# Optimization experiments

Hardware: AMD Instinct MI355X
Metric: run time of the kernel (lower is better)

Reference implementation:

```python
import jax, jax.numpy as jnp
import numpy as np

B, S, D = 2, 2048, 2048
H, KVH = 32, 8
HD = D // H          # 64
N_REP = H // KVH     # 4
NEG = -1e9


def setup_inputs() -> dict:
    key = jax.random.key(0)
    ks = jax.random.split(key, 5)
    x = jax.random.normal(ks[0], (B, S, D), dtype=jnp.float32)
    std = 0.02
    wq = jax.random.normal(ks[1], (H * HD, D), dtype=jnp.float32) * std
    wk = jax.random.normal(ks[2], (KVH * HD, D), dtype=jnp.float32) * std
    wv = jax.random.normal(ks[3], (KVH * HD, D), dtype=jnp.float32) * std
    wo = jax.random.normal(ks[4], (D, H * HD), dtype=jnp.float32) * std
    # RoPE tables: (S, HD//2)
    inv_freq = 1.0 / (10000.0 ** (np.arange(0, HD, 2, dtype=np.float32) / HD))
    t = np.arange(S, dtype=np.float32)
    freqs = np.outer(t, inv_freq)
    freqs_cos = jnp.asarray(np.cos(freqs))
    freqs_sin = jnp.asarray(np.sin(freqs))
    # additive causal mask [1,1,S,S]
    causal = np.tril(np.ones((S, S), dtype=bool))
    mask = jnp.asarray(np.where(causal, 0.0, NEG).astype(np.float32))[None, None]
    return {"x": x, "wq": wq, "wk": wk, "wv": wv, "wo": wo,
            "freqs_cos": freqs_cos, "freqs_sin": freqs_sin, "mask": mask}


def _apply_rope(t, cos, sin):
    # t: [B,S,nh,HD]; cos/sin: [S, HD//2]
    tr = t.reshape(t.shape[:-1] + (HD // 2, 2))
    r, i = tr[..., 0], tr[..., 1]
    c = cos[None, :, None, :]
    s = sin[None, :, None, :]
    out_r = r * c - i * s
    out_i = r * s + i * c
    return jnp.stack([out_r, out_i], axis=-1).reshape(t.shape)


def reference(x, wq, wk, wv, wo, freqs_cos, freqs_sin, mask):
    b, s, _ = x.shape
    q = (x @ wq.T).reshape(b, s, H, HD)
    k = (x @ wk.T).reshape(b, s, KVH, HD)
    v = (x @ wv.T).reshape(b, s, KVH, HD)
    q = _apply_rope(q, freqs_cos, freqs_sin)
    k = _apply_rope(k, freqs_cos, freqs_sin)
    # repeat_kv (GQA expansion) then move heads forward: [B,H,S,HD]
    k = jnp.repeat(k, N_REP, axis=2)
    v = jnp.repeat(v, N_REP, axis=2)
    q = q.transpose(0, 2, 1, 3)
    k = k.transpose(0, 2, 1, 3)
    v = v.transpose(0, 2, 1, 3)
    scale = 1.0 / jnp.sqrt(jnp.float32(HD))
    scores = jnp.einsum("bhqd,bhkd->bhqk", q, k) * scale + mask[:, :, :s, :s]
    attn = jax.nn.softmax(scores, axis=-1)
    out = jnp.einsum("bhqk,bhkd->bhqd", attn, v)
    out = out.transpose(0, 2, 1, 3).reshape(b, s, H * HD)
    return out @ wo.T
```

## Files before the change

### kernel.cpp

```cpp
#include <hip/hip_runtime.h>
#include <hip/hip_bf16.h>
#include <stdint.h>


#define NEG_BIG (-1e9f)
#define SCALE_LOG2 0.18033688011112042f

typedef __bf16 bf16x8 __attribute__((ext_vector_type(8)));
typedef float f32x4 __attribute__((ext_vector_type(4)));
typedef float f32x16 __attribute__((ext_vector_type(16)));
typedef uint16_t u16x8 __attribute__((ext_vector_type(8)));
typedef uint32_t u32x4 __attribute__((ext_vector_type(4)));

__device__ inline uint16_t f2bf(float x) {
    __hip_bfloat16 h = __float2bfloat16(x);
    return __builtin_bit_cast(uint16_t, h);
}
__device__ inline float bf2f(uint16_t u) {
    uint32_t t = (uint32_t)u << 16;
    return __builtin_bit_cast(float, t);
}

__device__ inline void async_cp16(const void* g, void* l) {
    __builtin_amdgcn_global_load_lds(
        (const __attribute__((address_space(1))) uint32_t*)g,
        (__attribute__((address_space(3))) uint32_t*)l,
        16 , 0 , 0 );
}

__global__ void cvt4(const float* __restrict__ in, uint16_t* __restrict__ out, int n4) {
    int i = blockIdx.x * blockDim.x + threadIdx.x;
    if (i >= n4) return;
    const float4 v = ((const float4*)in)[i];
    ushort4 o;
    o.x = f2bf(v.x); o.y = f2bf(v.y); o.z = f2bf(v.z); o.w = f2bf(v.w);
    ((ushort4*)out)[i] = o;
}

__global__ void build_wqkv(const float* __restrict__ wq, const float* __restrict__ wk,
                           const float* __restrict__ wv, uint16_t* __restrict__ out) {
    int i = blockIdx.x * blockDim.x + threadIdx.x;
    if (i >= (3072 * 2048) / 4) return;
    int e = i * 4;
    int row = e >> 11;
    int col = e & 2047;
    const float* src = (row < 2048) ? (wq + (long)row * 2048 + col)
                     : (row < 2560) ? (wk + (long)(row - 2048) * 2048 + col)
                                    : (wv + (long)(row - 2560) * 2048 + col);
    const float4 v = *(const float4*)src;
    ushort4 o;
    o.x = f2bf(v.x); o.y = f2bf(v.y); o.z = f2bf(v.z); o.w = f2bf(v.w);
    ((ushort4*)(out + e))[0] = o;
}

template <int OUT_BF16>
__global__ __launch_bounds__(256) void gemm_bt(const uint16_t* __restrict__ A,
                                               const uint16_t* __restrict__ Bw,
                                               void* __restrict__ Cout,
                                               int M, int N, int K) {
    __shared__ __align__(16) uint16_t Asm[128 * 32];
    __shared__ __align__(16) uint16_t Bsm[128 * 32];
    const int t = threadIdx.x;
    const int l = t & 63;
    const int w = t >> 6;
    const int wr = w >> 1, wc = w & 1;
    const int c = l & 15, g = l >> 4;
    const long row0 = (long)blockIdx.x * 128;
    const long col0 = (long)blockIdx.y * 128;

    f32x4 acc[4][4] = {};

    const uint16_t* aSrc = A + (row0 + (t >> 2)) * (long)K + (t & 3) * 8;
    const uint16_t* bSrc = Bw + (col0 + (t >> 2)) * (long)K + (t & 3) * 8;
    const long half = 64L * K;

    for (int k0 = 0; k0 < K; k0 += 32) {
        __syncthreads();
        async_cp16(aSrc + k0, &Asm[t * 8]);
        async_cp16(aSrc + half + k0, &Asm[2048 + t * 8]);
        async_cp16(bSrc + k0, &Bsm[t * 8]);
        async_cp16(bSrc + half + k0, &Bsm[2048 + t * 8]);
        __syncthreads();

        bf16x8 aF[4], bF[4];
        const int ko = g * 8;
#pragma unroll
        for (int m = 0; m < 4; ++m)
            aF[m] = *(const bf16x8*)&Asm[(wr * 64 + m * 16 + c) * 32 + ko];
#pragma unroll
        for (int n = 0; n < 4; ++n)
            bF[n] = *(const bf16x8*)&Bsm[(wc * 64 + n * 16 + c) * 32 + ko];
#pragma unroll
        for (int m = 0; m < 4; ++m)
#pragma unroll
            for (int n = 0; n < 4; ++n)
                acc[m][n] = __builtin_amdgcn_mfma_f32_16x16x32_bf16(aF[m], bF[n], acc[m][n], 0, 0, 0);
    }

#pragma unroll
    for (int m = 0; m < 4; ++m) {
        const long rg = row0 + wr * 64 + m * 16 + g * 4;
#pragma unroll
        for (int n = 0; n < 4; ++n) {
            const long cg = col0 + wc * 64 + n * 16 + c;
#pragma unroll
            for (int r = 0; r < 4; ++r) {
                float v = acc[m][n][r];
                if (OUT_BF16)
                    ((uint16_t*)Cout)[(rg + r) * (long)N + cg] = f2bf(v);
                else
                    ((float*)Cout)[(rg + r) * (long)N + cg] = v;
            }
        }
    }
}

__global__ void rope_inplace(uint16_t* __restrict__ qkv,
                             const float* __restrict__ cosT,
                             const float* __restrict__ sinT) {
    const int PPR = 1280;
    int idx = blockIdx.x * blockDim.x + threadIdx.x;
    if (idx >= 4096 * PPR) return;
    int m = idx / PPR;
    int j = idx - m * PPR;
    int col = (j < 1024) ? (2 * j) : (2048 + 2 * (j - 1024));
    int s = m & 2047;
    int d2 = j & 31;
    float cc = cosT[s * 32 + d2];
    float ss = sinT[s * 32 + d2];
    uint32_t* p = (uint32_t*)(qkv + (long)m * 3072 + col);
    uint32_t v = *p;
    float re = bf2f((uint16_t)(v & 0xffffu));
    float im = bf2f((uint16_t)(v >> 16));
    float orr = re * cc - im * ss;
    float oi = re * ss + im * cc;
    *p = (uint32_t)f2bf(orr) | ((uint32_t)f2bf(oi) << 16);
}

__global__ void pack_vt(const uint16_t* __restrict__ qkv, uint16_t* __restrict__ Vt) {
    const int wid = (blockIdx.x * blockDim.x + threadIdx.x) >> 6;
    const int lane = threadIdx.x & 63;
    const int head = wid >> 8;
    const int sblk = wid & 255;
    const int b = head >> 3, kvh = head & 7;
    const uint16_t* src = qkv + ((long)(b * 2048 + sblk * 8)) * 3072 + 2560 + kvh * 64 + lane;
    u16x8 v;
#pragma unroll
    for (int j = 0; j < 8; ++j) v[j] = src[(long)j * 3072];
    uint16_t* dst = Vt + ((long)head * 64 + lane) * 2048 + sblk * 8;
    *(u16x8*)dst = v;
}

__global__ void kpack(const uint16_t* __restrict__ qkv, uint16_t* __restrict__ Kpk) {
    const int wid = (blockIdx.x * blockDim.x + threadIdx.x) >> 6;
    const int l = threadIdx.x & 63;
    const int lq = l & 31, hi = l >> 5;
    const int s = wid & 3;
    const int tile = (wid >> 2) & 63;
    const int bk = wid >> 8;
    const int b = bk >> 3, kvh = bk & 7;
    const uint16_t* src = qkv + (long)(b * 2048 + 32 * tile + lq) * 3072
                        + 2048 + kvh * 64 + 16 * s + 8 * hi;
    u16x8 v = *(const u16x8*)src;
    *(u16x8*)(Kpk + (((long)(bk * 64 + tile) * 4 + s) * 64 + l) * 8) = v;
}

__global__ void vpack2(const uint16_t* __restrict__ Vt, uint16_t* __restrict__ Vpk) {
    const int wid = (blockIdx.x * blockDim.x + threadIdx.x) >> 6;
    const int l = threadIdx.x & 63;
    const int lq = l & 31, hi = l >> 5;
    const int s2 = wid & 1;
    const int nd = (wid >> 1) & 1;
    const int tile = (wid >> 2) & 63;
    const int bk = wid >> 8;
    const uint16_t* src = Vt + ((long)(bk * 64 + nd * 32 + lq)) * 2048
                        + 32 * tile + 16 * s2 + 8 * hi;
    u16x8 v = *(const u16x8*)src;
    *(u16x8*)(Vpk + ((((long)(bk * 64 + tile) * 2 + nd) * 2 + s2) * 64 + l) * 8) = v;
}

__global__ __launch_bounds__(128, 4) void attn_fwd(const uint16_t* __restrict__ qkv,
                                                   const uint16_t* __restrict__ Kpk,
                                                   const uint16_t* __restrict__ Vpk,
                                                   uint16_t* __restrict__ outb) {
    const int bid = blockIdx.x;
    const int bhp = bid & 31;
    const int j = 63 - (bid >> 5);
    const int t = threadIdx.x;
    const int l = t & 63, ww = t >> 6;
    const int gh = 2 * bhp + ww;
    const int b = gh >> 5, h = gh & 31;
    const int kvh = h >> 2;
    const int bk = b * 8 + kvh;
    const int lq = l & 31, hi = l >> 5;
    const int q = 32 * j + lq;

    const uint16_t* qrow = qkv + (long)(b * 2048 + q) * 3072 + h * 64 + 8 * hi;
    bf16x8 qf[4];
#pragma unroll
    for (int s = 0; s < 4; ++s) qf[s] = *(const bf16x8*)(qrow + 16 * s);

    float m_run = -1e30f, l_run = 0.f;
    f32x16 accO[2] = {};

    const uint16_t* kbase = Kpk + (long)bk * 64 * 2048 + (long)l * 8;
    const uint16_t* vbase = Vpk + (long)bk * 64 * 2048 + (long)l * 8;
    const int ntiles = j + 1;

    for (int tile = 0; tile < ntiles; ++tile) {
        const uint16_t* kp = kbase + (long)tile * 2048;
        bf16x8 kf[4];
#pragma unroll
        for (int s = 0; s < 4; ++s) kf[s] = *(const bf16x8*)(kp + s * 512);

        f32x16 st = {};
#pragma unroll
        for (int s = 0; s < 4; ++s)
            st = __builtin_amdgcn_mfma_f32_32x32x16_bf16(kf[s], qf[s], st, 0, 0, 0);

        const uint16_t* vp = vbase + (long)tile * 2048;
        bf16x8 vf[2][2];
#pragma unroll
        for (int nd = 0; nd < 2; ++nd)
#pragma unroll
            for (int s2 = 0; s2 < 2; ++s2)
                vf[nd][s2] = *(const bf16x8*)(vp + nd * 1024 + s2 * 512);

        float sc[16];
        if (tile == j) {
            const int tq = lq - 4 * hi;
#pragma unroll
            for (int r = 0; r < 16; ++r) {
                const int kc = (r & 3) + 8 * (r >> 2);
                sc[r] = st[r] * SCALE_LOG2 + (kc > tq ? NEG_BIG : 0.f);
            }
        } else {
#pragma unroll
            for (int r = 0; r < 16; ++r) sc[r] = st[r] * SCALE_LOG2;
        }

        float vm = sc[0];
#pragma unroll
        for (int r = 1; r < 16; ++r) vm = fmaxf(vm, sc[r]);
        vm = fmaxf(vm, __shfl_xor(vm, 32));
        const float mnew = fmaxf(m_run, vm);
        const float alpha = __builtin_amdgcn_exp2f(m_run - mnew);
        m_run = mnew;

        float pr[16];
        float sum = 0.f;
#pragma unroll
        for (int r = 0; r < 16; ++r) {
            pr[r] = __builtin_amdgcn_exp2f(sc[r] - mnew);
            sum += pr[r];
        }
        sum += __shfl_xor(sum, 32);
        l_run = l_run * alpha + sum;

        uint32_t wds[8], xw[8];
#pragma unroll
        for (int m = 0; m < 8; ++m)
            wds[m] = (uint32_t)f2bf(pr[2 * m]) | ((uint32_t)f2bf(pr[2 * m + 1]) << 16);
#pragma unroll
        for (int m = 0; m < 8; ++m)
            xw[m] = (uint32_t)__shfl_xor((int)wds[m], 32);

        bf16x8 pf[2];
#pragma unroll
        for (int s = 0; s < 2; ++s) {
            u32x4 pk;
            pk[0] = hi ? xw[4 * s + 2] : wds[4 * s + 0];
            pk[1] = hi ? xw[4 * s + 3] : wds[4 * s + 1];
            pk[2] = hi ? wds[4 * s + 2] : xw[4 * s + 0];
            pk[3] = hi ? wds[4 * s + 3] : xw[4 * s + 1];
            pf[s] = __builtin_bit_cast(bf16x8, pk);
        }

#pragma unroll
        for (int nd = 0; nd < 2; ++nd)
#pragma unroll
            for (int r = 0; r < 16; ++r) accO[nd][r] *= alpha;
#pragma unroll
        for (int nd = 0; nd < 2; ++nd)
#pragma unroll
            for (int s = 0; s < 2; ++s)
                accO[nd] = __builtin_amdgcn_mfma_f32_32x32x16_bf16(vf[nd][s], pf[s], accO[nd], 0, 0, 0);
    }

    const float invl = 1.0f / l_run;
    uint16_t* orow = outb + (long)(b * 2048 + q) * 2048 + h * 64 + 4 * hi;
#pragma unroll
    for (int nd = 0; nd < 2; ++nd)
#pragma unroll
        for (int m = 0; m < 4; ++m) {
            ushort4 o;
            o.x = f2bf(accO[nd][4 * m + 0] * invl);
            o.y = f2bf(accO[nd][4 * m + 1] * invl);
            o.z = f2bf(accO[nd][4 * m + 2] * invl);
            o.w = f2bf(accO[nd][4 * m + 3] * invl);
            *(ushort4*)(orow + nd * 32 + 8 * m) = o;
        }
}

extern "C" void kernel_launch(void* const* d_in, const int* in_sizes, int n_in,
                              void* d_out, int out_size, void* d_ws, size_t ws_size,
                              hipStream_t stream) {
    const float* x    = (const float*)d_in[0];
    const float* wq   = (const float*)d_in[1];
    const float* wk   = (const float*)d_in[2];
    const float* wv   = (const float*)d_in[3];
    const float* wo   = (const float*)d_in[4];
    const float* fcos = (const float*)d_in[5];
    const float* fsin = (const float*)d_in[6];
    float* out = (float*)d_out;

    uint8_t* ws = (uint8_t*)d_ws;
    const size_t MiB = 1048576;
    uint16_t* x_bf   = (uint16_t*)(ws);
    uint16_t* w_bf   = (uint16_t*)(ws + 16 * MiB);
    uint16_t* qkv_bf = (uint16_t*)(ws + 28 * MiB);
    uint16_t* att_bf = x_bf;
    uint16_t* Kpk    = (uint16_t*)(ws + 16 * MiB);
    uint16_t* Vpk    = (uint16_t*)(ws + 20 * MiB);
    uint16_t* Vt     = (uint16_t*)(ws + 24 * MiB);
    uint16_t* wo_bf  = (uint16_t*)(ws + 16 * MiB);

    cvt4<<<(2097152 + 255) / 256, 256, 0, stream>>>(x, x_bf, 2097152);
    build_wqkv<<<(1572864 + 255) / 256, 256, 0, stream>>>(wq, wk, wv, w_bf);

    gemm_bt<1><<<dim3(32, 24), 256, 0, stream>>>(x_bf, w_bf, qkv_bf, 4096, 3072, 2048);

    rope_inplace<<<(4096 * 1280 + 255) / 256, 256, 0, stream>>>(qkv_bf, fcos, fsin);

    pack_vt<<<1024, 256, 0, stream>>>(qkv_bf, Vt);
    kpack<<<1024, 256, 0, stream>>>(qkv_bf, Kpk);
    vpack2<<<1024, 256, 0, stream>>>(Vt, Vpk);

    attn_fwd<<<2048, 128, 0, stream>>>(qkv_bf, Kpk, Vpk, att_bf);

    cvt4<<<(1048576 + 255) / 256, 256, 0, stream>>>(wo, wo_bf, 1048576);
    gemm_bt<0><<<dim3(32, 16), 256, 0, stream>>>(att_bf, wo_bf, out, 4096, 2048, 2048);
}
```

Baseline: 236.7 us.

## Fuse K RoPE into packing, pack V directly, unroll attention two tiles with deferred rescale

K RoPE now runs inside the K packing kernel and V is packed straight from the qkv buffer, which drops the Vt intermediate and one launch. The attention loop handles two 32-key tiles per iteration and raises MFMA wave priority with s_setprio. It skips the online-softmax rescale unless the new max exceeds the running max by a threshold. The unroll raises register pressure, and the launch_bounds occupancy hint is removed. The deferred rescale lets exponentials reach up to 2^10 before the bf16 cast, which may shift precision.

```diff
diff --git a/kernel.cpp b/kernel.cpp
--- a/kernel.cpp
+++ b/kernel.cpp
@@ -5,6 +5,7 @@
 
 #define NEG_BIG (-1e9f)
 #define SCALE_LOG2 0.18033688011112042f
+#define DEFER_THR 10.0f
 
 typedef __bf16 bf16x8 __attribute__((ext_vector_type(8)));
 typedef float f32x4 __attribute__((ext_vector_type(4)));
@@ -115,20 +116,18 @@
     }
 }
 
-__global__ void rope_inplace(uint16_t* __restrict__ qkv,
-                             const float* __restrict__ cosT,
-                             const float* __restrict__ sinT) {
-    const int PPR = 1280;
+__global__ void rope_q(uint16_t* __restrict__ qkv,
+                       const float* __restrict__ cosT,
+                       const float* __restrict__ sinT) {
     int idx = blockIdx.x * blockDim.x + threadIdx.x;
-    if (idx >= 4096 * PPR) return;
-    int m = idx / PPR;
-    int j = idx - m * PPR;
-    int col = (j < 1024) ? (2 * j) : (2048 + 2 * (j - 1024));
+    if (idx >= 4096 * 1024) return;
+    int m = idx >> 10;
+    int j = idx & 1023;
     int s = m & 2047;
     int d2 = j & 31;
     float cc = cosT[s * 32 + d2];
     float ss = sinT[s * 32 + d2];
-    uint32_t* p = (uint32_t*)(qkv + (long)m * 3072 + col);
+    uint32_t* p = (uint32_t*)(qkv + (long)m * 3072 + 2 * j);
     uint32_t v = *p;
     float re = bf2f((uint16_t)(v & 0xffffu));
     float im = bf2f((uint16_t)(v >> 16));
@@ -137,21 +136,10 @@
     *p = (uint32_t)f2bf(orr) | ((uint32_t)f2bf(oi) << 16);
 }
 
-__global__ void pack_vt(const uint16_t* __restrict__ qkv, uint16_t* __restrict__ Vt) {
-    const int wid = (blockIdx.x * blockDim.x + threadIdx.x) >> 6;
-    const int lane = threadIdx.x & 63;
-    const int head = wid >> 8;
-    const int sblk = wid & 255;
-    const int b = head >> 3, kvh = head & 7;
-    const uint16_t* src = qkv + ((long)(b * 2048 + sblk * 8)) * 3072 + 2560 + kvh * 64 + lane;
-    u16x8 v;
-#pragma unroll
-    for (int j = 0; j < 8; ++j) v[j] = src[(long)j * 3072];
-    uint16_t* dst = Vt + ((long)head * 64 + lane) * 2048 + sblk * 8;
-    *(u16x8*)dst = v;
-}
-
-__global__ void kpack(const uint16_t* __restrict__ qkv, uint16_t* __restrict__ Kpk) {
+__global__ void kpack_rope(const uint16_t* __restrict__ qkv,
+                           const float* __restrict__ cosT,
+                           const float* __restrict__ sinT,
+                           uint16_t* __restrict__ Kpk) {
     const int wid = (blockIdx.x * blockDim.x + threadIdx.x) >> 6;
     const int l = threadIdx.x & 63;
     const int lq = l & 31, hi = l >> 5;
@@ -159,13 +147,25 @@
     const int tile = (wid >> 2) & 63;
     const int bk = wid >> 8;
     const int b = bk >> 3, kvh = bk & 7;
-    const uint16_t* src = qkv + (long)(b * 2048 + 32 * tile + lq) * 3072
+    const int key = 32 * tile + lq;
+    const uint16_t* src = qkv + (long)(b * 2048 + key) * 3072
                         + 2048 + kvh * 64 + 16 * s + 8 * hi;
     u16x8 v = *(const u16x8*)src;
-    *(u16x8*)(Kpk + (((long)(bk * 64 + tile) * 4 + s) * 64 + l) * 8) = v;
-}
-
-__global__ void vpack2(const uint16_t* __restrict__ Vt, uint16_t* __restrict__ Vpk) {
+    const int d2b = 8 * s + 4 * hi;
+    u16x8 o;
+#pragma unroll
+    for (int p = 0; p < 4; ++p) {
+        const float cc = cosT[key * 32 + d2b + p];
+        const float ss = sinT[key * 32 + d2b + p];
+        const float re = bf2f(v[2 * p]);
+        const float im = bf2f(v[2 * p + 1]);
+        o[2 * p]     = f2bf(re * cc - im * ss);
+        o[2 * p + 1] = f2bf(re * ss + im * cc);
+    }
+    *(u16x8*)(Kpk + (((long)(bk * 64 + tile) * 4 + s) * 64 + l) * 8) = o;
+}
+
+__global__ void vpack_direct(const uint16_t* __restrict__ qkv, uint16_t* __restrict__ Vpk) {
     const int wid = (blockIdx.x * blockDim.x + threadIdx.x) >> 6;
     const int l = threadIdx.x & 63;
     const int lq = l & 31, hi = l >> 5;
@@ -173,21 +173,44 @@
     const int nd = (wid >> 1) & 1;
     const int tile = (wid >> 2) & 63;
     const int bk = wid >> 8;
-    const uint16_t* src = Vt + ((long)(bk * 64 + nd * 32 + lq)) * 2048
-                        + 32 * tile + 16 * s2 + 8 * hi;
-    u16x8 v = *(const u16x8*)src;
+    const int b = bk >> 3, kvh = bk & 7;
+    const int key0 = 32 * tile + 16 * s2 + 8 * hi;
+    const uint16_t* src = qkv + (long)(b * 2048 + key0) * 3072
+                        + 2560 + kvh * 64 + nd * 32 + lq;
+    u16x8 v;
+#pragma unroll
+    for (int jj = 0; jj < 8; ++jj) v[jj] = src[(long)jj * 3072];
     *(u16x8*)(Vpk + ((((long)(bk * 64 + tile) * 2 + nd) * 2 + s2) * 64 + l) * 8) = v;
 }
 
-__global__ __launch_bounds__(128, 4) void attn_fwd(const uint16_t* __restrict__ qkv,
-                                                   const uint16_t* __restrict__ Kpk,
-                                                   const uint16_t* __restrict__ Vpk,
-                                                   uint16_t* __restrict__ outb) {
+__device__ inline void pack_pf(const float pr[16], int hi, bf16x8 pf[2]) {
+    uint32_t wds[8], xw[8];
+#pragma unroll
+    for (int m = 0; m < 8; ++m)
+        wds[m] = (uint32_t)f2bf(pr[2 * m]) | ((uint32_t)f2bf(pr[2 * m + 1]) << 16);
+#pragma unroll
+    for (int m = 0; m < 8; ++m)
+        xw[m] = (uint32_t)__shfl_xor((int)wds[m], 32);
+#pragma unroll
+    for (int s = 0; s < 2; ++s) {
+        u32x4 pk;
+        pk[0] = hi ? xw[4 * s + 2] : wds[4 * s + 0];
+        pk[1] = hi ? xw[4 * s + 3] : wds[4 * s + 1];
+        pk[2] = hi ? wds[4 * s + 2] : xw[4 * s + 0];
+        pk[3] = hi ? wds[4 * s + 3] : xw[4 * s + 1];
+        pf[s] = __builtin_bit_cast(bf16x8, pk);
+    }
+}
+
+__global__ __launch_bounds__(128) void attn_fwd(const uint16_t* __restrict__ qkv,
+                                                const uint16_t* __restrict__ Kpk,
+                                                const uint16_t* __restrict__ Vpk,
+                                                uint16_t* __restrict__ outb) {
     const int bid = blockIdx.x;
     const int bhp = bid & 31;
     const int j = 63 - (bid >> 5);
-    const int t = threadIdx.x;
-    const int l = t & 63, ww = t >> 6;
+    const int t0 = threadIdx.x;
+    const int l = t0 & 63, ww = t0 >> 6;
     const int gh = 2 * bhp + ww;
     const int b = gh >> 5, h = gh & 31;
     const int kvh = h >> 2;
@@ -205,86 +228,98 @@
 
     const uint16_t* kbase = Kpk + (long)bk * 64 * 2048 + (long)l * 8;
     const uint16_t* vbase = Vpk + (long)bk * 64 * 2048 + (long)l * 8;
-    const int ntiles = j + 1;
-
-    for (int tile = 0; tile < ntiles; ++tile) {
-        const uint16_t* kp = kbase + (long)tile * 2048;
-        bf16x8 kf[4];
-#pragma unroll
-        for (int s = 0; s < 4; ++s) kf[s] = *(const bf16x8*)(kp + s * 512);
-
-        f32x16 st = {};
+    const int nT = (j + 2) >> 1;
+
+    for (int t = 0; t < nT; ++t) {
+        bf16x8 kf[2][4];
+#pragma unroll
+        for (int u = 0; u < 2; ++u)
+#pragma unroll
+            for (int s = 0; s < 4; ++s)
+                kf[u][s] = *(const bf16x8*)(kbase + (long)(2 * t + u) * 2048 + s * 512);
+
+        f32x16 st0 = {}, st1 = {};
+        __builtin_amdgcn_s_setprio(1);
 #pragma unroll
         for (int s = 0; s < 4; ++s)
-            st = __builtin_amdgcn_mfma_f32_32x32x16_bf16(kf[s], qf[s], st, 0, 0, 0);
-
-        const uint16_t* vp = vbase + (long)tile * 2048;
-        bf16x8 vf[2][2];
-#pragma unroll
-        for (int nd = 0; nd < 2; ++nd)
-#pragma unroll
-            for (int s2 = 0; s2 < 2; ++s2)
-                vf[nd][s2] = *(const bf16x8*)(vp + nd * 1024 + s2 * 512);
-
-        float sc[16];
-        if (tile == j) {
-            const int tq = lq - 4 * hi;
+            st0 = __builtin_amdgcn_mfma_f32_32x32x16_bf16(kf[0][s], qf[s], st0, 0, 0, 0);
+#pragma unroll
+        for (int s = 0; s < 4; ++s)
+            st1 = __builtin_amdgcn_mfma_f32_32x32x16_bf16(kf[1][s], qf[s], st1, 0, 0, 0);
+        __builtin_amdgcn_s_setprio(0);
+
+        bf16x8 vf[2][2][2];
+#pragma unroll
+        for (int u = 0; u < 2; ++u)
+#pragma unroll
+            for (int nd = 0; nd < 2; ++nd)
+#pragma unroll
+                for (int s2 = 0; s2 < 2; ++s2)
+                    vf[u][nd][s2] = *(const bf16x8*)(vbase + (long)(2 * t + u) * 2048 + nd * 1024 + s2 * 512);
+
+        float sc0[16], sc1[16];
+        if (t == nT - 1) {
+            const int tq0 = lq + ((j - 2 * t) << 5) - 4 * hi;
+            const int tq1 = tq0 - 32;
 #pragma unroll
             for (int r = 0; r < 16; ++r) {
                 const int kc = (r & 3) + 8 * (r >> 2);
-                sc[r] = st[r] * SCALE_LOG2 + (kc > tq ? NEG_BIG : 0.f);
+                sc0[r] = st0[r] * SCALE_LOG2 + (kc > tq0 ? NEG_BIG : 0.f);
+                sc1[r] = st1[r] * SCALE_LOG2 + (kc > tq1 ? NEG_BIG : 0.f);
             }
         } else {
 #pragma unroll
-            for (int r = 0; r < 16; ++r) sc[r] = st[r] * SCALE_LOG2;
-        }
-
-        float vm = sc[0];
-#pragma unroll
-        for (int r = 1; r < 16; ++r) vm = fmaxf(vm, sc[r]);
+            for (int r = 0; r < 16; ++r) {
+                sc0[r] = st0[r] * SCALE_LOG2;
+                sc1[r] = st1[r] * SCALE_LOG2;
+            }
+        }
+
+        float vm = sc0[0];
+#pragma unroll
+        for (int r = 1; r < 16; ++r) vm = fmaxf(vm, sc0[r]);
+#pragma unroll
+        for (int r = 0; r < 16; ++r) vm = fmaxf(vm, sc1[r]);
         vm = fmaxf(vm, __shfl_xor(vm, 32));
-        const float mnew = fmaxf(m_run, vm);
-        const float alpha = __builtin_amdgcn_exp2f(m_run - mnew);
-        m_run = mnew;
-
-        float pr[16];
+        if (!__all(vm - m_run <= DEFER_THR)) {
+            const float mnew = fmaxf(m_run, vm);
+            const float alpha = __builtin_amdgcn_exp2f(m_run - mnew);
+            m_run = mnew;
+            l_run *= alpha;
+#pragma unroll
+            for (int nd = 0; nd < 2; ++nd)
+#pragma unroll
+                for (int r = 0; r < 16; ++r) accO[nd][r] *= alpha;
+        }
+
+        float pr0[16], pr1[16];
         float sum = 0.f;
 #pragma unroll
         for (int r = 0; r < 16; ++r) {
-            pr[r] = __builtin_amdgcn_exp2f(sc[r] - mnew);
-            sum += pr[r];
+            pr0[r] = __builtin_amdgcn_exp2f(sc0[r] - m_run);
+            sum += pr0[r];
+        }
+#pragma unroll
+        for (int r = 0; r < 16; ++r) {
+            pr1[r] = __builtin_amdgcn_exp2f(sc1[r] - m_run);
+            sum += pr1[r];
         }
         sum += __shfl_xor(sum, 32);
-        l_run = l_run * alpha + sum;
-
-        uint32_t wds[8], xw[8];
-#pragma unroll
-        for (int m = 0; m < 8; ++m)
-            wds[m] = (uint32_t)f2bf(pr[2 * m]) | ((uint32_t)f2bf(pr[2 * m + 1]) << 16);
-#pragma unroll
-        for (int m = 0; m < 8; ++m)
-            xw[m] = (uint32_t)__shfl_xor((int)wds[m], 32);
-
-        bf16x8 pf[2];
-#pragma unroll
-        for (int s = 0; s < 2; ++s) {
-            u32x4 pk;
-            pk[0] = hi ? xw[4 * s + 2] : wds[4 * s + 0];
-            pk[1] = hi ? xw[4 * s + 3] : wds[4 * s + 1];
-            pk[2] = hi ? wds[4 * s + 2] : xw[4 * s + 0];
-            pk[3] = hi ? wds[4 * s + 3] : xw[4 * s + 1];
-            pf[s] = __builtin_bit_cast(bf16x8, pk);
-        }
-
-#pragma unroll
-        for (int nd = 0; nd < 2; ++nd)
-#pragma unroll
-            for (int r = 0; r < 16; ++r) accO[nd][r] *= alpha;
-#pragma unroll
-        for (int nd = 0; nd < 2; ++nd)
-#pragma unroll
-            for (int s = 0; s < 2; ++s)
-                accO[nd] = __builtin_amdgcn_mfma_f32_32x32x16_bf16(vf[nd][s], pf[s], accO[nd], 0, 0, 0);
+        l_run += sum;
+
+        bf16x8 pf0[2], pf1[2];
+        pack_pf(pr0, hi, pf0);
+        pack_pf(pr1, hi, pf1);
+
+        __builtin_amdgcn_s_setprio(1);
+#pragma unroll
+        for (int nd = 0; nd < 2; ++nd) {
+            accO[nd] = __builtin_amdgcn_mfma_f32_32x32x16_bf16(vf[0][nd][0], pf0[0], accO[nd], 0, 0, 0);
+            accO[nd] = __builtin_amdgcn_mfma_f32_32x32x16_bf16(vf[0][nd][1], pf0[1], accO[nd], 0, 0, 0);
+            accO[nd] = __builtin_amdgcn_mfma_f32_32x32x16_bf16(vf[1][nd][0], pf1[0], accO[nd], 0, 0, 0);
+            accO[nd] = __builtin_amdgcn_mfma_f32_32x32x16_bf16(vf[1][nd][1], pf1[1], accO[nd], 0, 0, 0);
+        }
+        __builtin_amdgcn_s_setprio(0);
     }
 
     const float invl = 1.0f / l_run;
@@ -322,7 +357,6 @@
     uint16_t* att_bf = x_bf;
     uint16_t* Kpk    = (uint16_t*)(ws + 16 * MiB);
     uint16_t* Vpk    = (uint16_t*)(ws + 20 * MiB);
-    uint16_t* Vt     = (uint16_t*)(ws + 24 * MiB);
     uint16_t* wo_bf  = (uint16_t*)(ws + 16 * MiB);
 
     cvt4<<<(2097152 + 255) / 256, 256, 0, stream>>>(x, x_bf, 2097152);
@@ -330,11 +364,9 @@
 
     gemm_bt<1><<<dim3(32, 24), 256, 0, stream>>>(x_bf, w_bf, qkv_bf, 4096, 3072, 2048);
 
-    rope_inplace<<<(4096 * 1280 + 255) / 256, 256, 0, stream>>>(qkv_bf, fcos, fsin);
-
-    pack_vt<<<1024, 256, 0, stream>>>(qkv_bf, Vt);
-    kpack<<<1024, 256, 0, stream>>>(qkv_bf, Kpk);
-    vpack2<<<1024, 256, 0, stream>>>(Vt, Vpk);
+    rope_q<<<16384, 256, 0, stream>>>(qkv_bf, fcos, fsin);
+    kpack_rope<<<1024, 256, 0, stream>>>(qkv_bf, fcos, fsin, Kpk);
+    vpack_direct<<<1024, 256, 0, stream>>>(qkv_bf, Vpk);
 
     attn_fwd<<<2048, 128, 0, stream>>>(qkv_bf, Kpk, Vpk, att_bf);
 
```

New measurement: 230.6 us. 2.6% less time.
